# Performance work log

Measured on AMD Instinct MI355X. Metric: run time of the kernel, lower is better.

## Reference

```python
import jax, jax.numpy as jnp
import numpy as np
from jax import lax

NUM_CLASSES = 91
C_FEAT = 2048
HF = WF = 16          # backbone feature map size (512px image / stride 32)
STRIDE = 32           # anchor stride, as in source generate_base_anchors
N_ANCHOR_TYPES = 9
NMS_THR = 0.5
K_ROIS = 100          # fixed proposal count after NMS (padded, jit-safe)
SPATIAL_SCALE = 1.0 / 16.0
POOL = 7
SR = 2                # sampling ratio (source uses adaptive -1; fixed here)


def conv2d(x, w, b, pad):
    y = lax.conv_general_dilated(x, w, (1, 1), pad,
                                 dimension_numbers=('NCHW', 'OIHW', 'NCHW'))
    return y + b[None, :, None, None]


def setup_inputs():
    key = jax.random.key(0)
    ks = jax.random.split(key, 16)
    f32 = jnp.float32
    def w(k, shape, s=0.01):
        return jax.random.normal(k, shape, f32) * s
    z = lambda n: jnp.zeros((n,), f32)
    D = C_FEAT * POOL * POOL  # 100352
    return dict(
        x=jax.random.normal(ks[0], (1, C_FEAT, HF, WF), f32),
        rpn_w=w(ks[1], (512, C_FEAT, 3, 3)), rpn_b=z(512),
        cls_w=w(ks[2], (18, 512, 1, 1)), cls_b=z(18),
        bbox_w=w(ks[3], (36, 512, 1, 1)), bbox_b=z(36),
        fc1c_w=w(ks[4], (D, 4096)), fc1c_b=z(4096),
        fc2c_w=w(ks[5], (4096, NUM_CLASSES)), fc2c_b=z(NUM_CLASSES),
        fc1b_w=w(ks[6], (D, 4096)), fc1b_b=z(4096),
        fc2b_w=w(ks[7], (4096, 4)), fc2b_b=z(4),
        m1_w=w(ks[8], (256, C_FEAT, 3, 3)), m1_b=z(256),
        mt_w=w(ks[9], (256, 256, 2, 2)), mt_b=z(256),  # ConvT weight [C_in,C_out,kh,kw]
        m2_w=w(ks[10], (1, 256, 1, 1)), m2_b=z(1),
    )


def _anchors(hf, wf):
    scales = jnp.array([8.0, 16.0, 32.0])
    ratios = jnp.array([0.5, 1.0, 2.0])
    ws = (scales[:, None] * jnp.sqrt(ratios)[None, :]).reshape(-1)  # scale-major, 9
    hs = (scales[:, None] / jnp.sqrt(ratios)[None, :]).reshape(-1)
    base = jnp.stack([-ws / 2, -hs / 2, ws / 2, hs / 2], axis=1)    # [9,4]
    sy, sx = jnp.meshgrid(jnp.arange(hf) * STRIDE, jnp.arange(wf) * STRIDE, indexing='ij')
    shifts = jnp.stack([sx, sy, sx, sy], -1).reshape(-1, 4).astype(jnp.float32)  # [HW,4]
    return (base[:, None, :] + shifts[None, :, :]).reshape(-1, 4)   # [9*HW,4] anchor-type major


def _decode(a, d):
    wa = a[:, 2] - a[:, 0]
    ha = a[:, 3] - a[:, 1]
    cx = a[:, 0] + 0.5 * wa
    cy = a[:, 1] + 0.5 * ha
    px = cx + d[:, 0] * wa
    py = cy + d[:, 1] * ha
    pw = jnp.exp(d[:, 2]) * wa
    ph = jnp.exp(d[:, 3]) * ha
    return jnp.stack([px - 0.5 * pw, py - 0.5 * ph, px + 0.5 * pw, py + 0.5 * ph], 1)


def _nms_topk(boxes, scores, thr, k):
    n = boxes.shape[0]
    order = jnp.argsort(-scores)
    b = boxes[order]
    s = scores[order]
    area = (b[:, 2] - b[:, 0]) * (b[:, 3] - b[:, 1])
    xx1 = jnp.maximum(b[:, None, 0], b[None, :, 0])
    yy1 = jnp.maximum(b[:, None, 1], b[None, :, 1])
    xx2 = jnp.minimum(b[:, None, 2], b[None, :, 2])
    yy2 = jnp.minimum(b[:, None, 3], b[None, :, 3])
    inter = jnp.clip(xx2 - xx1, 0) * jnp.clip(yy2 - yy1, 0)
    iou = inter / (area[:, None] + area[None, :] - inter + 1e-9)
    j = jnp.arange(n)
    def body(i, keep):
        sup = keep[i] & (iou[i] > thr) & (j > i)
        return keep & ~sup
    keep = lax.fori_loop(0, n, body, jnp.ones((n,), bool))
    masked = jnp.where(keep, s, -jnp.inf)
    vals, pos = lax.top_k(masked, k)
    valid = jnp.isfinite(vals)
    fb = jnp.where(valid[:, None], b[pos], 0.0)
    fs = jnp.where(valid, vals, 0.0)
    return fb, fs


def _roi_align(feat, boxes):
    # feat: [C,H,W]; boxes: [K,4] in image coords
    C, H, W = feat.shape
    r = boxes * SPATIAL_SCALE
    S = POOL * SR  # 14 sample points per side
    t = (jnp.arange(S, dtype=feat.dtype) + 0.5) / S
    gx = jnp.clip(r[:, 0:1] + t[None, :] * (r[:, 2:3] - r[:, 0:1]), 0.0, W - 1.0)
    gy = jnp.clip(r[:, 1:2] + t[None, :] * (r[:, 3:4] - r[:, 1:2]), 0.0, H - 1.0)
    x0 = jnp.floor(gx); y0 = jnp.floor(gy)
    lx = gx - x0; ly = gy - y0
    x0i = x0.astype(jnp.int32); y0i = y0.astype(jnp.int32)
    x1i = jnp.minimum(x0i + 1, W - 1); y1i = jnp.minimum(y0i + 1, H - 1)
    flat = feat.reshape(C, H * W)
    def g(yi, xi):  # yi:[K,S] row coords, xi:[K,S] col coords -> [C,K,S,S]
        idx = yi[:, :, None] * W + xi[:, None, :]
        return flat[:, idx]
    lyb = ly[:, :, None]; lxb = lx[:, None, :]
    v = ((1 - lyb) * (1 - lxb) * g(y0i, x0i)
         + (1 - lyb) * lxb * g(y0i, x1i)
         + lyb * (1 - lxb) * g(y1i, x0i)
         + lyb * lxb * g(y1i, x1i))  # [C,K,S,S]
    v = v.reshape(C, -1, POOL, SR, POOL, SR).mean(axis=(3, 5))
    return v.transpose(1, 0, 2, 3)  # [K,C,7,7]


def reference(x, rpn_w, rpn_b, cls_w, cls_b, bbox_w, bbox_b,
              fc1c_w, fc1c_b, fc2c_w, fc2c_b,
              fc1b_w, fc1b_b, fc2b_w, fc2b_b,
              m1_w, m1_b, mt_w, mt_b, m2_w, m2_b):
    p1 = [(1, 1), (1, 1)]; p0 = [(0, 0), (0, 0)]
    f = jax.nn.relu(conv2d(x, rpn_w, rpn_b, p1))      # [1,512,H,W]
    obj = conv2d(f, cls_w, cls_b, p0)                 # [1,18,H,W]
    deltas = conv2d(f, bbox_w, bbox_b, p0)            # [1,36,H,W]
    hf, wf = f.shape[2], f.shape[3]
    hw = hf * wf
    # softmax over the 2 objectness classes (view(B,2,-1) layout)
    scores = jax.nn.softmax(obj.reshape(2, N_ANCHOR_TYPES, hw), axis=0)[1].reshape(-1)
    d = deltas.reshape(N_ANCHOR_TYPES, 4, hw).transpose(0, 2, 1).reshape(-1, 4)
    anchors = _anchors(hf, wf)
    boxes = _decode(anchors, d)
    fb, fs = _nms_topk(boxes, scores, NMS_THR, K_ROIS)
    rois = _roi_align(x[0], fb)                       # [K,2048,7,7]
    flat = rois.reshape(K_ROIS, -1)
    cls_out = jax.nn.relu(flat @ fc1c_w + fc1c_b) @ fc2c_w + fc2c_b
    box_out = jax.nn.relu(flat @ fc1b_w + fc1b_b) @ fc2b_w + fc2b_b
    m = jax.nn.relu(conv2d(rois, m1_w, m1_b, p1))     # [K,256,7,7]
    # ConvTranspose2d(k=2,s=2): non-overlapping, each pixel expands to a 2x2 block
    up = jnp.einsum('nchw,coij->nohiwj', m, mt_w).reshape(K_ROIS, 256, 2 * POOL, 2 * POOL)
    m = jax.nn.relu(up + mt_b[None, :, None, None])
    masks = conv2d(m, m2_w, m2_b, p0)                 # [K,1,14,14]
    return cls_out, box_out, masks
```

## Files before the change

### kernel.cpp

```cpp
#include <hip/hip_runtime.h>

#define DEVFN __device__ __forceinline__

typedef unsigned short ushort_t;
typedef unsigned int uint32;
typedef __attribute__((ext_vector_type(8))) short bf16x8;
typedef __attribute__((ext_vector_type(4))) float f32x4;

typedef __attribute__((address_space(3))) unsigned int lds_uint;
typedef const __attribute__((address_space(1))) unsigned int glob_uint;

DEVFN ushort_t f2bf(float x) {
    uint32 b = __float_as_uint(x);
    uint32 r = (b + 0x7FFFu + ((b >> 16) & 1u)) >> 16;
    return (ushort_t)r;
}
DEVFN float bf2f(ushort_t u) { return __uint_as_float(((uint32)u) << 16); }

union BWU { uint32 u[4]; bf16x8 v8; };

__global__ __launch_bounds__(256) void k_prep(const float* __restrict__ m1_w,
                                              const float* __restrict__ mt_w,
                                              const float* __restrict__ x,
                                              ushort_t* __restrict__ wAf,
                                              ushort_t* __restrict__ wA2f,
                                              float* __restrict__ xt) {
    const int bid = blockIdx.x, tid = threadIdx.x;
    if (bid < 256) {
        const int p = bid * 4 + (tid >> 6);
        const int lane = tid & 63, l15 = lane & 15, lg = lane >> 4;
        const int cot = p >> 6, cis = p & 63;
        const int co = cot * 16 + l15, k0 = cis * 32 + lg * 8;
        const float* src = m1_w + ((size_t)co * 2048 + k0) * 9;
        float v[72];
#pragma unroll
        for (int i = 0; i < 72; ++i) v[i] = src[i];
#pragma unroll
        for (int tap = 0; tap < 9; ++tap) {
            ushort_t* dst = wAf + ((size_t)((tap * 16 + cot) * 64 + cis) * 512) + lane * 8;
            ushort_t t8[8];
#pragma unroll
            for (int j = 0; j < 8; ++j) t8[j] = f2bf(v[j * 9 + tap]);
            uint4 u;
            u.x = (uint32)t8[0] | ((uint32)t8[1] << 16);
            u.y = (uint32)t8[2] | ((uint32)t8[3] << 16);
            u.z = (uint32)t8[4] | ((uint32)t8[5] << 16);
            u.w = (uint32)t8[6] | ((uint32)t8[7] << 16);
            *(uint4*)dst = u;
        }
    } else if (bid < 1280) {
        int idx = (bid - 256) * 256 + tid;
        int j = idx & 7, lane = (idx >> 3) & 63, cis = (idx >> 9) & 7, cot = idx >> 12;
        int row = cot * 16 + (lane & 15);
        int c = cis * 32 + (lane >> 4) * 8 + j;
        int o = row >> 2, ij = row & 3;
        wA2f[idx] = f2bf(mt_w[((size_t)c * 256 + o) * 4 + ij]);
    } else {
        int pos = bid - 1280;
        for (int i = 0; i < 8; ++i) {
            int c = tid + i * 256;
            xt[(size_t)pos * 2048 + c] = x[(size_t)c * 256 + pos];
        }
    }
}

__global__ __launch_bounds__(256) void k_rpn(const float* __restrict__ x,
                                             const float* __restrict__ rpn_w,
                                             float* __restrict__ fpart) {
    __shared__ float xs[8][18][18];
    const int coP = blockIdx.x, ks = blockIdx.y, tid = threadIdx.x;
    const int ty = tid >> 4, tx = tid & 15;
    const int co0 = coP * 4;
    for (int i = tid; i < 8 * 18 * 18; i += 256) ((float*)xs)[i] = 0.f;
    float acc[4] = {0.f, 0.f, 0.f, 0.f};
    for (int ch = 0; ch < 32; ++ch) {
        const int cib = ks * 256 + ch * 8;
        __syncthreads();
#pragma unroll
        for (int cc = 0; cc < 8; ++cc) xs[cc][ty + 1][tx + 1] = x[(size_t)(cib + cc) * 256 + tid];
        __syncthreads();
#pragma unroll
        for (int cc = 0; cc < 8; ++cc) {
            const int ci = cib + cc;
            float v[9];
#pragma unroll
            for (int t = 0; t < 9; ++t) v[t] = xs[cc][ty + t / 3][tx + t % 3];
            const float* wb = rpn_w + ((size_t)co0 * 2048 + ci) * 9;
#pragma unroll
            for (int o = 0; o < 4; ++o) {
                const float* w = wb + (size_t)o * 2048 * 9;
#pragma unroll
                for (int t = 0; t < 9; ++t) acc[o] = fmaf(v[t], w[t], acc[o]);
            }
        }
    }
#pragma unroll
    for (int o = 0; o < 4; ++o) fpart[((size_t)ks * 512 + co0 + o) * 256 + tid] = acc[o];
}

__global__ void k_rpn_reduce(const float* __restrict__ fpart, const float* __restrict__ rpn_b,
                             float* __restrict__ f) {
    const int i = blockIdx.x * 256 + threadIdx.x;
    float s = 0.f;
#pragma unroll
    for (int p = 0; p < 8; ++p) s += fpart[(size_t)p * 131072 + i];
    f[i] = fmaxf(s + rpn_b[i >> 8], 0.f);
}

__global__ void k_head(const float* __restrict__ f, const float* __restrict__ cls_w,
                       const float* __restrict__ cls_b, const float* __restrict__ bbox_w,
                       const float* __restrict__ bbox_b, float* __restrict__ scores,
                       float* __restrict__ boxes) {
    const int a = blockIdx.x, pos = threadIdx.x;
    float o0 = 0, o1 = 0, d0 = 0, d1 = 0, d2 = 0, d3 = 0;
    const float* c0 = cls_w + (size_t)a * 512;
    const float* c1 = cls_w + (size_t)(9 + a) * 512;
    const float* b0p = bbox_w + (size_t)(4 * a) * 512;
    const float* b1p = b0p + 512;
    const float* b2p = b0p + 1024;
    const float* b3p = b0p + 1536;
    for (int ci = 0; ci < 512; ci += 8) {
        float fv[8];
#pragma unroll
        for (int j = 0; j < 8; ++j) fv[j] = f[(size_t)(ci + j) * 256 + pos];
#pragma unroll
        for (int j = 0; j < 8; ++j) {
            o0 = fmaf(c0[ci + j], fv[j], o0);
            o1 = fmaf(c1[ci + j], fv[j], o1);
            d0 = fmaf(b0p[ci + j], fv[j], d0);
            d1 = fmaf(b1p[ci + j], fv[j], d1);
            d2 = fmaf(b2p[ci + j], fv[j], d2);
            d3 = fmaf(b3p[ci + j], fv[j], d3);
        }
    }
    o0 += cls_b[a]; o1 += cls_b[9 + a];
    d0 += bbox_b[4 * a + 0]; d1 += bbox_b[4 * a + 1];
    d2 += bbox_b[4 * a + 2]; d3 += bbox_b[4 * a + 3];
    float mx = fmaxf(o0, o1);
    float e0 = expf(o0 - mx), e1 = expf(o1 - mx);
    float sc = e1 / (e0 + e1);
    int si = a / 3, ri = a % 3;
    float scale = (si == 0) ? 8.f : ((si == 1) ? 16.f : 32.f);
    float ratio = (ri == 0) ? 0.5f : ((ri == 1) ? 1.f : 2.f);
    float sq = sqrtf(ratio);
    float hw2 = (scale * sq) * 0.5f;
    float hh2 = (scale / sq) * 0.5f;
    int py = pos >> 4, px = pos & 15;
    float sx = (float)(px * 32), sy = (float)(py * 32);
    float a0 = sx - hw2, a1 = sy - hh2, a2 = sx + hw2, a3 = sy + hh2;
    float wa = a2 - a0, ha = a3 - a1;
    float cx = a0 + 0.5f * wa, cy = a1 + 0.5f * ha;
    float pxc = cx + d0 * wa, pyc = cy + d1 * ha;
    float pw = expf(d2) * wa, ph = expf(d3) * ha;
    int idx = a * 256 + pos;
    scores[idx] = sc;
    boxes[idx * 4 + 0] = pxc - 0.5f * pw;
    boxes[idx * 4 + 1] = pyc - 0.5f * ph;
    boxes[idx * 4 + 2] = pxc + 0.5f * pw;
    boxes[idx * 4 + 3] = pyc + 0.5f * ph;
}

__global__ void k_sort(const float* __restrict__ scores, const float* __restrict__ boxes,
                       float* __restrict__ ssort, float* __restrict__ bsort) {
    const int i = blockIdx.x * 256 + threadIdx.x;
    const float si = scores[i];
    int rank = 0;
    for (int j = 0; j < 2304; ++j) {
        float sj = scores[j];
        rank += (sj > si) || (sj == si && j < i);
    }
    ssort[rank] = si;
    float4 bb = *(const float4*)(boxes + (size_t)i * 4);
    *(float4*)(bsort + (size_t)rank * 4) = bb;
}

__global__ void k_adj(const float* __restrict__ bsort, unsigned long long* __restrict__ adj) {
    const int i = blockIdx.x, lane = threadIdx.x;
    const float4 bi = *(const float4*)(bsort + (size_t)i * 4);
    const float ai = (bi.z - bi.x) * (bi.w - bi.y);
    for (int w = 0; w < 36; ++w) {
        int j = w * 64 + lane;
        bool sup = false;
        if (j < 2304 && j > i) {
            float4 bj = *(const float4*)(bsort + (size_t)j * 4);
            float aj = (bj.z - bj.x) * (bj.w - bj.y);
            float xx1 = fmaxf(bi.x, bj.x), yy1 = fmaxf(bi.y, bj.y);
            float xx2 = fminf(bi.z, bj.z), yy2 = fminf(bi.w, bj.w);
            float inter = fmaxf(xx2 - xx1, 0.f) * fmaxf(yy2 - yy1, 0.f);
            float iou = inter / (ai + aj - inter + 1e-9f);
            sup = iou > 0.5f;
        }
        unsigned long long m = __ballot(sup);
        if (lane == 0) adj[(size_t)i * 36 + w] = m;
    }
}

__global__ void k_nms(const unsigned long long* __restrict__ adj, const float* __restrict__ bsort,
                      float* __restrict__ fb) {
    const int lane = threadIdx.x;
    unsigned long long r = (lane < 36) ? 0ULL : ~0ULL;
    int cnt = 0;
    for (int it = 0; it < 128; ++it) {
        unsigned long long inv = ~r;
        int local = inv ? (__ffsll((unsigned long long)inv) - 1) : 64;
        int cand = (local < 64) ? lane * 64 + local : (1 << 30);
#pragma unroll
        for (int d = 32; d; d >>= 1) cand = min(cand, __shfl_xor(cand, d));
        if (cand >= 2304) break;
        if (lane == 0) *(float4*)(fb + (size_t)cnt * 4) = *(const float4*)(bsort + (size_t)cand * 4);
        ++cnt;
        if (cnt == 100) break;
        unsigned long long a = (lane < 36) ? adj[(size_t)cand * 36 + lane] : 0ULL;
        r |= a;
        if (lane == (cand >> 6)) r |= 1ULL << (cand & 63);
    }
    for (int s2 = lane; s2 < 100; s2 += 64)
        if (s2 >= cnt) {
            float4 z = {0.f, 0.f, 0.f, 0.f};
            *(float4*)(fb + (size_t)s2 * 4) = z;
        }
}

__global__ __launch_bounds__(256) void k_roi(const float* __restrict__ xt,
                                             const float* __restrict__ fb,
                                             ushort_t* __restrict__ flatA,
                                             ushort_t* __restrict__ flatT) {
    __shared__ int sxi0[14], sxi1[14], syi0[14], syi1[14];
    __shared__ float slx[14], sly[14];
    const int cg = blockIdx.x, n = blockIdx.y, tid = threadIdx.x;
    const float r0 = fb[n * 4 + 0] * 0.0625f, r1 = fb[n * 4 + 1] * 0.0625f;
    const float r2 = fb[n * 4 + 2] * 0.0625f, r3 = fb[n * 4 + 3] * 0.0625f;
    if (tid < 14) {
        float tt = ((float)tid + 0.5f) * (1.0f / 14.0f);
        float gx = r0 + tt * (r2 - r0);
        gx = fminf(fmaxf(gx, 0.f), 15.f);
        float x0f = floorf(gx);
        int x0 = (int)x0f;
        sxi0[tid] = x0; sxi1[tid] = min(x0 + 1, 15); slx[tid] = gx - x0f;
        float gy = r1 + tt * (r3 - r1);
        gy = fminf(fmaxf(gy, 0.f), 15.f);
        float y0f = floorf(gy);
        int y0 = (int)y0f;
        syi0[tid] = y0; syi1[tid] = min(y0 + 1, 15); sly[tid] = gy - y0f;
    }
    __syncthreads();
    const int c = cg * 256 + tid;
    for (int py = 0; py < 7; ++py) {
        for (int px = 0; px < 7; ++px) {
            float accv = 0.f;
#pragma unroll
            for (int a2 = 0; a2 < 2; ++a2) {
                int sy = py * 2 + a2;
                int y0 = syi0[sy], y1 = syi1[sy];
                float ly = sly[sy];
#pragma unroll
                for (int b2 = 0; b2 < 2; ++b2) {
                    int sx = px * 2 + b2;
                    int x0 = sxi0[sx], x1 = sxi1[sx];
                    float lx = slx[sx];
                    float v00 = xt[(size_t)(y0 * 16 + x0) * 2048 + c];
                    float v01 = xt[(size_t)(y0 * 16 + x1) * 2048 + c];
                    float v10 = xt[(size_t)(y1 * 16 + x0) * 2048 + c];
                    float v11 = xt[(size_t)(y1 * 16 + x1) * 2048 + c];
                    accv += (1.f - ly) * (1.f - lx) * v00 + (1.f - ly) * lx * v01 +
                            ly * (1.f - lx) * v10 + ly * lx * v11;
                }
            }
            ushort_t bv = f2bf(accv * 0.25f);
            int pos = py * 7 + px;
            flatT[((size_t)n * 49 + pos) * 2048 + c] = bv;
            int k = c * 49 + pos;
            flatA[((size_t)(k >> 5) * 112 + n) * 32 + (k & 31)] = bv;
        }
    }
}

__global__ __launch_bounds__(256, 4) void k_big(const ushort_t* __restrict__ flatA,
                                                const ushort_t* __restrict__ flatT,
                                                const float* __restrict__ Wc,
                                                const float* __restrict__ Wb,
                                                float* __restrict__ part,
                                                const ushort_t* __restrict__ wAf,
                                                const float* __restrict__ m1_b,
                                                ushort_t* __restrict__ m1outT) {
    __shared__ float wlds[2][32][128];
    const int bid = blockIdx.x, tid = threadIdx.x;
    const int wave = tid >> 6, lane = tid & 63, l15 = lane & 15, lg = lane >> 4;
    const f32x4 zz = {0.f, 0.f, 0.f, 0.f};
    if (bid < 77) {
        const int nb = bid;
        int nn[4], ppy[4], ppx[4], colv[4];
#pragma unroll
        for (int nt = 0; nt < 4; ++nt) {
            int col = nb * 64 + nt * 16 + l15;
            colv[nt] = col;
            int n = col / 49;
            int pos = col - n * 49;
            nn[nt] = n;
            ppy[nt] = pos / 7;
            ppx[nt] = pos - (pos / 7) * 7;
        }
        f32x4 acc[4][4];
#pragma unroll
        for (int a = 0; a < 4; ++a)
#pragma unroll
            for (int b = 0; b < 4; ++b) acc[a][b] = zz;
        bf16x8 zfrag;
#pragma unroll
        for (int j = 0; j < 8; ++j) zfrag[j] = 0;
        for (int tap = 0; tap < 9; ++tap) {
            const int ty = tap / 3 - 1, tx = tap % 3 - 1;
            int val[4];
            size_t bofs[4];
#pragma unroll
            for (int nt = 0; nt < 4; ++nt) {
                int iy = ppy[nt] + ty, ix = ppx[nt] + tx;
                val[nt] = (iy >= 0 && iy < 7 && ix >= 0 && ix < 7);
                bofs[nt] = ((size_t)nn[nt] * 49 + iy * 7 + ix) * 2048;
            }
            for (int cis = 0; cis < 64; ++cis) {
                const int kq = cis * 32 + lg * 8;
                bf16x8 a[4];
#pragma unroll
                for (int mt = 0; mt < 4; ++mt)
                    a[mt] = *(const bf16x8*)(wAf +
                            ((size_t)((tap * 16 + wave * 4 + mt) * 64 + cis) * 64 + lane) * 8);
                bf16x8 b[4];
#pragma unroll
                for (int nt = 0; nt < 4; ++nt)
                    b[nt] = val[nt] ? *(const bf16x8*)(flatT + bofs[nt] + kq) : zfrag;
#pragma unroll
                for (int nt = 0; nt < 4; ++nt)
#pragma unroll
                    for (int mt = 0; mt < 4; ++mt)
                        acc[mt][nt] = __builtin_amdgcn_mfma_f32_16x16x32_bf16(a[mt], b[nt], acc[mt][nt], 0, 0, 0);
            }
        }
#pragma unroll
        for (int mt = 0; mt < 4; ++mt)
#pragma unroll
            for (int nt = 0; nt < 4; ++nt) {
                int co0 = wave * 64 + mt * 16 + lg * 4;
                ushort_t v[4];
#pragma unroll
                for (int r = 0; r < 4; ++r)
                    v[r] = f2bf(fmaxf(acc[mt][nt][r] + m1_b[co0 + r], 0.f));
                uint2 u;
                u.x = (uint32)v[0] | ((uint32)v[1] << 16);
                u.y = (uint32)v[2] | ((uint32)v[3] << 16);
                *(uint2*)(m1outT + (size_t)colv[nt] * 256 + co0) = u;
            }
        return;
    }
    const int h = bid - 77;
    const int x = h & 7, t = h >> 3;
    const int colTile = t >> 2, rem = t & 3;
    const int kc = x * 2 + (rem & 1), br = rem >> 1;
    const float* W = br ? Wb : Wc;
    const int ncol0 = colTile * 128 + wave * 32;
    const int k0 = kc * 6272;
    const float* wbase = W + (size_t)k0 * 4096 + colTile * 128;
    const int srow = lane >> 5, scol = (lane & 31) * 4;

    auto stage = [&](int buf, int s) {
        const float* g0 = wbase + ((size_t)(s * 32 + wave * 8 + srow)) * 4096 + scol;
#pragma unroll
        for (int q = 0; q < 4; ++q) {
            const float* g = g0 + (size_t)(q * 2) * 4096;
            float* l = &wlds[buf][wave * 8 + q * 2][0];
            __builtin_amdgcn_global_load_lds((glob_uint*)g, (lds_uint*)l, 16, 0, 0);
        }
    };

    f32x4 acc0[7], acc1[7];
#pragma unroll
    for (int tt = 0; tt < 7; ++tt) { acc0[tt] = zz; acc1[tt] = zz; }

    stage(0, 0);
    __syncthreads();
    const ushort_t* ap = flatA + ((size_t)(kc * 196) * 112 + l15) * 32 + lg * 8;
    for (int s = 0; s < 196; ++s) {
        const int b = s & 1;
        if (s + 1 < 196) stage(b ^ 1, s + 1);
        bf16x8 af[7];
#pragma unroll
        for (int tt = 0; tt < 7; ++tt) af[tt] = *(const bf16x8*)(ap + (size_t)tt * 512);
        const float* wrow = &wlds[b][lg * 8][wave * 32 + l15];
        BWU b0u, b1u;
#pragma unroll
        for (int i = 0; i < 4; ++i) {
            float w0a = wrow[(2 * i) * 128], w0b = wrow[(2 * i + 1) * 128];
            float w1a = wrow[(2 * i) * 128 + 16], w1b = wrow[(2 * i + 1) * 128 + 16];
            asm("v_cvt_pk_bf16_f32 %0, %1, %2" : "=v"(b0u.u[i]) : "v"(w0a), "v"(w0b));
            asm("v_cvt_pk_bf16_f32 %0, %1, %2" : "=v"(b1u.u[i]) : "v"(w1a), "v"(w1b));
        }
#pragma unroll
        for (int tt = 0; tt < 7; ++tt) {
            acc0[tt] = __builtin_amdgcn_mfma_f32_16x16x32_bf16(af[tt], b0u.v8, acc0[tt], 0, 0, 0);
            acc1[tt] = __builtin_amdgcn_mfma_f32_16x16x32_bf16(af[tt], b1u.v8, acc1[tt], 0, 0, 0);
        }
        ap += 3584;
        __syncthreads();
    }
    float* pb = part + (size_t)(br * 16 + kc) * 112 * 4096;
#pragma unroll
    for (int tt = 0; tt < 7; ++tt)
#pragma unroll
        for (int r = 0; r < 4; ++r) {
            int m = tt * 16 + lg * 4 + r;
            pb[(size_t)m * 4096 + ncol0 + l15] = acc0[tt][r];
            pb[(size_t)m * 4096 + ncol0 + 16 + l15] = acc1[tt][r];
        }
}

__global__ __launch_bounds__(256) void k_fc2(const float* __restrict__ part,
                                             const float* __restrict__ fc1c_b,
                                             const float* __restrict__ fc1b_b,
                                             const float* __restrict__ Wc,
                                             const float* __restrict__ bc,
                                             const float* __restrict__ Wb,
                                             const float* __restrict__ bb,
                                             float* __restrict__ out) {
    __shared__ float h_s[2][4096];
    __shared__ float ph[2][91];
    __shared__ float pbx[2][4];
    const int m = blockIdx.x, tid = threadIdx.x;
    for (int i = tid; i < 8192; i += 256) {
        int br = i >> 12, col = i & 4095;
        float s = br ? fc1b_b[col] : fc1c_b[col];
#pragma unroll
        for (int p = 0; p < 16; ++p) s += part[((size_t)(br * 16 + p) * 112 + m) * 4096 + col];
        h_s[br][col] = fmaxf(s, 0.f);
    }
    __syncthreads();
    const int half = tid >> 7, col = tid & 127;
    if (col < 91) {
        const float* hrow = &h_s[0][half * 2048];
        const float* wp = Wc + (size_t)half * 2048 * 91 + col;
        float a0 = 0, a1 = 0, a2 = 0, a3 = 0, a4 = 0, a5 = 0, a6 = 0, a7 = 0;
        for (int k = 0; k < 2048; k += 8) {
            a0 = fmaf(hrow[k],     wp[(size_t)k * 91], a0);
            a1 = fmaf(hrow[k + 1], wp[(size_t)(k + 1) * 91], a1);
            a2 = fmaf(hrow[k + 2], wp[(size_t)(k + 2) * 91], a2);
            a3 = fmaf(hrow[k + 3], wp[(size_t)(k + 3) * 91], a3);
            a4 = fmaf(hrow[k + 4], wp[(size_t)(k + 4) * 91], a4);
            a5 = fmaf(hrow[k + 5], wp[(size_t)(k + 5) * 91], a5);
            a6 = fmaf(hrow[k + 6], wp[(size_t)(k + 6) * 91], a6);
            a7 = fmaf(hrow[k + 7], wp[(size_t)(k + 7) * 91], a7);
        }
        ph[half][col] = ((a0 + a1) + (a2 + a3)) + ((a4 + a5) + (a6 + a7));
    } else if (col >= 96 && col < 100) {
        int bcol = col - 96;
        const float* hrow = &h_s[1][half * 2048];
        const float* wp = Wb + (size_t)half * 2048 * 4 + bcol;
        float a0 = 0, a1 = 0, a2 = 0, a3 = 0, a4 = 0, a5 = 0, a6 = 0, a7 = 0;
        for (int k = 0; k < 2048; k += 8) {
            a0 = fmaf(hrow[k],     wp[(size_t)k * 4], a0);
            a1 = fmaf(hrow[k + 1], wp[(size_t)(k + 1) * 4], a1);
            a2 = fmaf(hrow[k + 2], wp[(size_t)(k + 2) * 4], a2);
            a3 = fmaf(hrow[k + 3], wp[(size_t)(k + 3) * 4], a3);
            a4 = fmaf(hrow[k + 4], wp[(size_t)(k + 4) * 4], a4);
            a5 = fmaf(hrow[k + 5], wp[(size_t)(k + 5) * 4], a5);
            a6 = fmaf(hrow[k + 6], wp[(size_t)(k + 6) * 4], a6);
            a7 = fmaf(hrow[k + 7], wp[(size_t)(k + 7) * 4], a7);
        }
        pbx[half][bcol] = ((a0 + a1) + (a2 + a3)) + ((a4 + a5) + (a6 + a7));
    }
    __syncthreads();
    if (tid < 91) out[m * 91 + tid] = bc[tid] + ph[0][tid] + ph[1][tid];
    else if (tid >= 96 && tid < 100) {
        int bcol = tid - 96;
        out[9100 + m * 4 + bcol] = bb[bcol] + pbx[0][bcol] + pbx[1][bcol];
    }
}

__global__ __launch_bounds__(256) void k_up(const ushort_t* __restrict__ m1outT,
                                            const ushort_t* __restrict__ wA2f,
                                            ushort_t* __restrict__ upT) {
    const int nb = blockIdx.x, cq = blockIdx.y, tid = threadIdx.x;
    const int wave = tid >> 6, lane = tid & 63, l15 = lane & 15, lg = lane >> 4;
    int colv[4];
#pragma unroll
    for (int nt = 0; nt < 4; ++nt) colv[nt] = nb * 64 + nt * 16 + l15;
    f32x4 acc[4][4];
    const f32x4 zz = {0.f, 0.f, 0.f, 0.f};
#pragma unroll
    for (int a = 0; a < 4; ++a)
#pragma unroll
        for (int b = 0; b < 4; ++b) acc[a][b] = zz;
    for (int cis = 0; cis < 8; ++cis) {
        const int kq = cis * 32 + lg * 8;
        bf16x8 a[4];
#pragma unroll
        for (int mt = 0; mt < 4; ++mt)
            a[mt] = *(const bf16x8*)(wA2f +
                    ((size_t)((cq * 16 + wave * 4 + mt) * 8 + cis) * 64 + lane) * 8);
        bf16x8 b[4];
#pragma unroll
        for (int nt = 0; nt < 4; ++nt)
            b[nt] = *(const bf16x8*)(m1outT + (size_t)colv[nt] * 256 + kq);
#pragma unroll
        for (int nt = 0; nt < 4; ++nt)
#pragma unroll
            for (int mt = 0; mt < 4; ++mt)
                acc[mt][nt] = __builtin_amdgcn_mfma_f32_16x16x32_bf16(a[mt], b[nt], acc[mt][nt], 0, 0, 0);
    }
#pragma unroll
    for (int mt = 0; mt < 4; ++mt)
#pragma unroll
        for (int nt = 0; nt < 4; ++nt) {
            int rb = (cq * 16 + wave * 4 + mt) * 16 + lg * 4;
            ushort_t v[4];
#pragma unroll
            for (int r = 0; r < 4; ++r) v[r] = f2bf(acc[mt][nt][r]);
            uint2 u;
            u.x = (uint32)v[0] | ((uint32)v[1] << 16);
            u.y = (uint32)v[2] | ((uint32)v[3] << 16);
            *(uint2*)(upT + (size_t)colv[nt] * 1024 + rb) = u;
        }
}

__global__ void k_mask(const ushort_t* __restrict__ upT, const float* __restrict__ mt_b,
                       const float* __restrict__ m2_w, const float* __restrict__ m2_b,
                       float* __restrict__ out) {
    const int n = blockIdx.x, t = threadIdx.x;
    if (t >= 196) return;
    const int ys = t / 14, xs = t % 14;
    const int ro = (ys & 1) * 2 + (xs & 1);
    const int col = n * 49 + (ys >> 1) * 7 + (xs >> 1);
    const ushort_t* up0 = upT + (size_t)col * 1024 + ro;
    float a0 = m2_b[0], a1 = 0.f, a2 = 0.f, a3 = 0.f;
#pragma unroll 4
    for (int o = 0; o < 256; o += 4) {
        a0 = fmaf(m2_w[o],     fmaxf(bf2f(up0[(o) * 4]) + mt_b[o], 0.f), a0);
        a1 = fmaf(m2_w[o + 1], fmaxf(bf2f(up0[(o + 1) * 4]) + mt_b[o + 1], 0.f), a1);
        a2 = fmaf(m2_w[o + 2], fmaxf(bf2f(up0[(o + 2) * 4]) + mt_b[o + 2], 0.f), a2);
        a3 = fmaf(m2_w[o + 3], fmaxf(bf2f(up0[(o + 3) * 4]) + mt_b[o + 3], 0.f), a3);
    }
    out[9500 + n * 196 + t] = (a0 + a1) + (a2 + a3);
}

extern "C" void kernel_launch(void* const* d_in, const int* in_sizes, int n_in,
                              void* d_out, int out_size, void* d_ws, size_t ws_size,
                              hipStream_t stream) {
    const float* x      = (const float*)d_in[0];
    const float* rpn_w  = (const float*)d_in[1];
    const float* rpn_b  = (const float*)d_in[2];
    const float* cls_w  = (const float*)d_in[3];
    const float* cls_b  = (const float*)d_in[4];
    const float* bbox_w = (const float*)d_in[5];
    const float* bbox_b = (const float*)d_in[6];
    const float* fc1c_w = (const float*)d_in[7];
    const float* fc1c_b = (const float*)d_in[8];
    const float* fc2c_w = (const float*)d_in[9];
    const float* fc2c_b = (const float*)d_in[10];
    const float* fc1b_w = (const float*)d_in[11];
    const float* fc1b_b = (const float*)d_in[12];
    const float* fc2b_w = (const float*)d_in[13];
    const float* fc2b_b = (const float*)d_in[14];
    const float* m1_w   = (const float*)d_in[15];
    const float* m1_b   = (const float*)d_in[16];
    const float* mt_w   = (const float*)d_in[17];
    const float* mt_b   = (const float*)d_in[18];
    const float* m2_w   = (const float*)d_in[19];
    const float* m2_b   = (const float*)d_in[20];
    float* out = (float*)d_out;

    char* ws = (char*)d_ws;
    size_t off = 0;
    auto take = [&](size_t nbytes) -> char* {
        char* p = ws + off;
        off += (nbytes + 255) & ~(size_t)255;
        return p;
    };
    float* xt      = (float*)take(2097152);
    float* fpart   = (float*)take(4194304);
    float* f       = (float*)take(524288);
    float* scores  = (float*)take(9216);
    float* boxes   = (float*)take(36864);
    float* ssort   = (float*)take(9216);
    float* bsort   = (float*)take(36864);
    unsigned long long* adj = (unsigned long long*)take(663552);
    float* fb      = (float*)take(1600);
    ushort_t* flatA = (ushort_t*)take(22478848);
    ushort_t* flatT = (ushort_t*)take(20471808);
    float* part1   = (float*)take(58720256);
    ushort_t* wAf  = (ushort_t*)take(9437184);
    ushort_t* m1outT = (ushort_t*)take(2523136);
    ushort_t* wA2f = (ushort_t*)take(524288);
    ushort_t* upT  = (ushort_t*)part1;

    k_prep<<<1536, 256, 0, stream>>>(m1_w, mt_w, x, wAf, wA2f, xt);
    k_rpn<<<dim3(128, 8), 256, 0, stream>>>(x, rpn_w, fpart);
    k_rpn_reduce<<<512, 256, 0, stream>>>(fpart, rpn_b, f);
    k_head<<<9, 256, 0, stream>>>(f, cls_w, cls_b, bbox_w, bbox_b, scores, boxes);
    k_sort<<<9, 256, 0, stream>>>(scores, boxes, ssort, bsort);
    k_adj<<<2304, 64, 0, stream>>>(bsort, adj);
    k_nms<<<1, 64, 0, stream>>>(adj, bsort, fb);
    k_roi<<<dim3(8, 100), 256, 0, stream>>>(xt, fb, flatA, flatT);
    k_big<<<1101, 256, 0, stream>>>(flatA, flatT, fc1c_w, fc1b_w, part1, wAf, m1_b, m1outT);
    k_fc2<<<100, 256, 0, stream>>>(part1, fc1c_b, fc1b_b, fc2c_w, fc2c_b, fc2b_w, fc2b_b, out);
    k_up<<<dim3(77, 4), 256, 0, stream>>>(m1outT, wA2f, upT);
    k_mask<<<100, 256, 0, stream>>>(upT, mt_b, m2_w, m2_b, out);
}
```

Baseline: 1.541 ms.

## Merge RPN conv into prep kernel and software-pipeline FC1 activation loads

The RPN conv kernel and the weight/transpose prep kernel become one launch, with block-index ranges selecting the role, which saves a launch and lets the two independent workloads overlap. In the FC1 GEMM loop of k_big, the next step's activation fragments are prefetched into registers alongside the LDS weight staging. Explicit vmcnt waits and raw s_barrier calls replace __syncthreads. The launch bound's min-blocks hint of 4 is dropped, so the compiler may use more registers and occupancy can fall.

```diff
diff --git a/kernel.cpp b/kernel.cpp
--- a/kernel.cpp
+++ b/kernel.cpp
@@ -19,15 +19,50 @@
 
 union BWU { uint32 u[4]; bf16x8 v8; };
 
-__global__ __launch_bounds__(256) void k_prep(const float* __restrict__ m1_w,
-                                              const float* __restrict__ mt_w,
-                                              const float* __restrict__ x,
-                                              ushort_t* __restrict__ wAf,
-                                              ushort_t* __restrict__ wA2f,
-                                              float* __restrict__ xt) {
+__global__ __launch_bounds__(256) void k_pre(const float* __restrict__ x,
+                                             const float* __restrict__ rpn_w,
+                                             float* __restrict__ fpart,
+                                             const float* __restrict__ m1_w,
+                                             const float* __restrict__ mt_w,
+                                             ushort_t* __restrict__ wAf,
+                                             ushort_t* __restrict__ wA2f,
+                                             float* __restrict__ xt) {
     const int bid = blockIdx.x, tid = threadIdx.x;
-    if (bid < 256) {
-        const int p = bid * 4 + (tid >> 6);
+    if (bid < 1024) {
+        __shared__ float xs[8][18][18];
+        const int coP = bid & 127, ks = bid >> 7;
+        const int ty = tid >> 4, tx = tid & 15;
+        const int co0 = coP * 4;
+        for (int i = tid; i < 8 * 18 * 18; i += 256) ((float*)xs)[i] = 0.f;
+        float acc[4] = {0.f, 0.f, 0.f, 0.f};
+        for (int ch = 0; ch < 32; ++ch) {
+            const int cib = ks * 256 + ch * 8;
+            __syncthreads();
+#pragma unroll
+            for (int cc = 0; cc < 8; ++cc) xs[cc][ty + 1][tx + 1] = x[(size_t)(cib + cc) * 256 + tid];
+            __syncthreads();
+#pragma unroll
+            for (int cc = 0; cc < 8; ++cc) {
+                const int ci = cib + cc;
+                float v[9];
+#pragma unroll
+                for (int t = 0; t < 9; ++t) v[t] = xs[cc][ty + t / 3][tx + t % 3];
+                const float* wb = rpn_w + ((size_t)co0 * 2048 + ci) * 9;
+#pragma unroll
+                for (int o = 0; o < 4; ++o) {
+                    const float* w = wb + (size_t)o * 2048 * 9;
+#pragma unroll
+                    for (int t = 0; t < 9; ++t) acc[o] = fmaf(v[t], w[t], acc[o]);
+                }
+            }
+        }
+#pragma unroll
+        for (int o = 0; o < 4; ++o) fpart[((size_t)ks * 512 + co0 + o) * 256 + tid] = acc[o];
+        return;
+    }
+    const int pb = bid - 1024;
+    if (pb < 256) {
+        const int p = pb * 4 + (tid >> 6);
         const int lane = tid & 63, l15 = lane & 15, lg = lane >> 4;
         const int cot = p >> 6, cis = p & 63;
         const int co = cot * 16 + l15, k0 = cis * 32 + lg * 8;
@@ -48,54 +83,20 @@
             u.w = (uint32)t8[6] | ((uint32)t8[7] << 16);
             *(uint4*)dst = u;
         }
-    } else if (bid < 1280) {
-        int idx = (bid - 256) * 256 + tid;
+    } else if (pb < 1280) {
+        int idx = (pb - 256) * 256 + tid;
         int j = idx & 7, lane = (idx >> 3) & 63, cis = (idx >> 9) & 7, cot = idx >> 12;
         int row = cot * 16 + (lane & 15);
         int c = cis * 32 + (lane >> 4) * 8 + j;
         int o = row >> 2, ij = row & 3;
         wA2f[idx] = f2bf(mt_w[((size_t)c * 256 + o) * 4 + ij]);
     } else {
-        int pos = bid - 1280;
+        int pos = pb - 1280;
         for (int i = 0; i < 8; ++i) {
             int c = tid + i * 256;
             xt[(size_t)pos * 2048 + c] = x[(size_t)c * 256 + pos];
         }
     }
-}
-
-__global__ __launch_bounds__(256) void k_rpn(const float* __restrict__ x,
-                                             const float* __restrict__ rpn_w,
-                                             float* __restrict__ fpart) {
-    __shared__ float xs[8][18][18];
-    const int coP = blockIdx.x, ks = blockIdx.y, tid = threadIdx.x;
-    const int ty = tid >> 4, tx = tid & 15;
-    const int co0 = coP * 4;
-    for (int i = tid; i < 8 * 18 * 18; i += 256) ((float*)xs)[i] = 0.f;
-    float acc[4] = {0.f, 0.f, 0.f, 0.f};
-    for (int ch = 0; ch < 32; ++ch) {
-        const int cib = ks * 256 + ch * 8;
-        __syncthreads();
-#pragma unroll
-        for (int cc = 0; cc < 8; ++cc) xs[cc][ty + 1][tx + 1] = x[(size_t)(cib + cc) * 256 + tid];
-        __syncthreads();
-#pragma unroll
-        for (int cc = 0; cc < 8; ++cc) {
-            const int ci = cib + cc;
-            float v[9];
-#pragma unroll
-            for (int t = 0; t < 9; ++t) v[t] = xs[cc][ty + t / 3][tx + t % 3];
-            const float* wb = rpn_w + ((size_t)co0 * 2048 + ci) * 9;
-#pragma unroll
-            for (int o = 0; o < 4; ++o) {
-                const float* w = wb + (size_t)o * 2048 * 9;
-#pragma unroll
-                for (int t = 0; t < 9; ++t) acc[o] = fmaf(v[t], w[t], acc[o]);
-            }
-        }
-    }
-#pragma unroll
-    for (int o = 0; o < 4; ++o) fpart[((size_t)ks * 512 + co0 + o) * 256 + tid] = acc[o];
 }
 
 __global__ void k_rpn_reduce(const float* __restrict__ fpart, const float* __restrict__ rpn_b,
@@ -275,14 +276,14 @@
     }
 }
 
-__global__ __launch_bounds__(256, 4) void k_big(const ushort_t* __restrict__ flatA,
-                                                const ushort_t* __restrict__ flatT,
-                                                const float* __restrict__ Wc,
-                                                const float* __restrict__ Wb,
-                                                float* __restrict__ part,
-                                                const ushort_t* __restrict__ wAf,
-                                                const float* __restrict__ m1_b,
-                                                ushort_t* __restrict__ m1outT) {
+__global__ __launch_bounds__(256) void k_big(const ushort_t* __restrict__ flatA,
+                                             const ushort_t* __restrict__ flatT,
+                                             const float* __restrict__ Wc,
+                                             const float* __restrict__ Wb,
+                                             float* __restrict__ part,
+                                             const ushort_t* __restrict__ wAf,
+                                             const float* __restrict__ m1_b,
+                                             ushort_t* __restrict__ m1outT) {
     __shared__ float wlds[2][32][128];
     const int bid = blockIdx.x, tid = threadIdx.x;
     const int wave = tid >> 6, lane = tid & 63, l15 = lane & 15, lg = lane >> 4;
@@ -358,8 +359,7 @@
     const int kc = x * 2 + (rem & 1), br = rem >> 1;
     const float* W = br ? Wb : Wc;
     const int ncol0 = colTile * 128 + wave * 32;
-    const int k0 = kc * 6272;
-    const float* wbase = W + (size_t)k0 * 4096 + colTile * 128;
+    const float* wbase = W + (size_t)(kc * 6272) * 4096 + colTile * 128;
     const int srow = lane >> 5, scol = (lane & 31) * 4;
 
     auto stage = [&](int buf, int s) {
@@ -376,15 +376,33 @@
 #pragma unroll
     for (int tt = 0; tt < 7; ++tt) { acc0[tt] = zz; acc1[tt] = zz; }
 
+    const ushort_t* ap = flatA + ((size_t)(kc * 196) * 112 + l15) * 32 + lg * 8;
     stage(0, 0);
-    __syncthreads();
-    const ushort_t* ap = flatA + ((size_t)(kc * 196) * 112 + l15) * 32 + lg * 8;
+    bf16x8 afc[7];
+#pragma unroll
+    for (int tt = 0; tt < 7; ++tt) afc[tt] = *(const bf16x8*)(ap + (size_t)tt * 512);
+    asm volatile("s_waitcnt vmcnt(0)" ::: "memory");
+    __builtin_amdgcn_sched_barrier(0);
+    __builtin_amdgcn_s_barrier();
+    __builtin_amdgcn_sched_barrier(0);
+
     for (int s = 0; s < 196; ++s) {
         const int b = s & 1;
-        if (s + 1 < 196) stage(b ^ 1, s + 1);
-        bf16x8 af[7];
-#pragma unroll
-        for (int tt = 0; tt < 7; ++tt) af[tt] = *(const bf16x8*)(ap + (size_t)tt * 512);
+        bf16x8 afn[7];
+        if (s + 1 < 196) {
+            const ushort_t* apn = ap + 3584;
+#pragma unroll
+            for (int tt = 0; tt < 7; ++tt) afn[tt] = *(const bf16x8*)(apn + (size_t)tt * 512);
+            stage(b ^ 1, s + 1);
+            asm volatile("s_waitcnt vmcnt(11)" ::: "memory");
+        } else {
+#pragma unroll
+            for (int tt = 0; tt < 7; ++tt) afn[tt] = afc[tt];
+            asm volatile("s_waitcnt vmcnt(0)" ::: "memory");
+        }
+        __builtin_amdgcn_sched_barrier(0);
+        __builtin_amdgcn_s_barrier();
+        __builtin_amdgcn_sched_barrier(0);
         const float* wrow = &wlds[b][lg * 8][wave * 32 + l15];
         BWU b0u, b1u;
 #pragma unroll
@@ -396,11 +414,15 @@
         }
 #pragma unroll
         for (int tt = 0; tt < 7; ++tt) {
-            acc0[tt] = __builtin_amdgcn_mfma_f32_16x16x32_bf16(af[tt], b0u.v8, acc0[tt], 0, 0, 0);
-            acc1[tt] = __builtin_amdgcn_mfma_f32_16x16x32_bf16(af[tt], b1u.v8, acc1[tt], 0, 0, 0);
-        }
+            acc0[tt] = __builtin_amdgcn_mfma_f32_16x16x32_bf16(afc[tt], b0u.v8, acc0[tt], 0, 0, 0);
+            acc1[tt] = __builtin_amdgcn_mfma_f32_16x16x32_bf16(afc[tt], b1u.v8, acc1[tt], 0, 0, 0);
+        }
+        __builtin_amdgcn_sched_barrier(0);
+        __builtin_amdgcn_s_barrier();
+        __builtin_amdgcn_sched_barrier(0);
+#pragma unroll
+        for (int tt = 0; tt < 7; ++tt) afc[tt] = afn[tt];
         ap += 3584;
-        __syncthreads();
     }
     float* pb = part + (size_t)(br * 16 + kc) * 112 * 4096;
 #pragma unroll
@@ -590,8 +612,7 @@
     ushort_t* wA2f = (ushort_t*)take(524288);
     ushort_t* upT  = (ushort_t*)part1;
 
-    k_prep<<<1536, 256, 0, stream>>>(m1_w, mt_w, x, wAf, wA2f, xt);
-    k_rpn<<<dim3(128, 8), 256, 0, stream>>>(x, rpn_w, fpart);
+    k_pre<<<2560, 256, 0, stream>>>(x, rpn_w, fpart, m1_w, mt_w, wAf, wA2f, xt);
     k_rpn_reduce<<<512, 256, 0, stream>>>(fpart, rpn_b, f);
     k_head<<<9, 256, 0, stream>>>(f, cls_w, cls_b, bbox_w, bbox_b, scores, boxes);
     k_sort<<<9, 256, 0, stream>>>(scores, boxes, ssort, bsort);
```

Result: faster. 1.487 ms (-3.5%).
